# Kernel optimization log

Measured on AMD Instinct MI355X. Metric: run time of the kernel, lower is better.

The kernel has to match this reference:

```python
import jax, jax.numpy as jnp
import numpy as np

DIM = 8          # per-head dim
ATT_EPS = 1e-15  # LiteMLA eps
BN_EPS = 1e-5    # torch BatchNorm2d default eps


def conv2d(x, w, groups=1, pad=0):
    # x: NCHW, w: OIHW
    return jax.lax.conv_general_dilated(
        x, w, window_strides=(1, 1), padding=[(pad, pad), (pad, pad)],
        dimension_numbers=('NCHW', 'OIHW', 'NCHW'), feature_group_count=groups)


def setup_inputs() -> dict:
    key = jax.random.key(0)
    ks = jax.random.split(key, 6)
    B, C, H, W = 4, 128, 128, 128
    heads = C // DIM            # 16
    t3 = 3 * C                  # 3*total_dim = 384
    x = jax.random.normal(ks[0], (B, C, H, W), jnp.float32)
    w_qkv = jax.random.normal(ks[1], (t3, C, 1, 1), jnp.float32) * 0.02
    w_dw = jax.random.normal(ks[2], (t3, 1, 5, 5), jnp.float32) * 0.02      # depthwise 5x5
    w_pw = jax.random.normal(ks[3], (t3, t3 // (3 * heads), 1, 1), jnp.float32) * 0.05  # grouped 1x1, groups=3*heads
    w_proj = jax.random.normal(ks[4], (C, 2 * C, 1, 1), jnp.float32) * 0.02  # proj 1x1: 2C -> C
    bn_gamma = jnp.ones((C,), jnp.float32)
    bn_beta = jnp.zeros((C,), jnp.float32)
    bn_mean = jnp.zeros((C,), jnp.float32)
    bn_var = jnp.ones((C,), jnp.float32)
    return dict(x=x, w_qkv=w_qkv, w_dw=w_dw, w_pw=w_pw, w_proj=w_proj,
                bn_gamma=bn_gamma, bn_beta=bn_beta, bn_mean=bn_mean, bn_var=bn_var)


def reference(x, w_qkv, w_dw, w_pw, w_proj, bn_gamma, bn_beta, bn_mean, bn_var):
    # qkv: 1x1 conv, no norm / no act
    qkv = conv2d(x, w_qkv)                                  # (B, 3C, H, W)
    t3 = w_qkv.shape[0]
    # aggreg[0]: depthwise 5x5 + grouped 1x1
    groups_pw = t3 // w_pw.shape[1]                         # 3*heads
    agg = conv2d(conv2d(qkv, w_dw, groups=t3, pad=2), w_pw, groups=groups_pw)
    qkv = jnp.concatenate([qkv, agg], axis=1)               # (B, 6C, H, W)

    B, _, H, W = qkv.shape
    N = H * W
    qkv = qkv.reshape(B, -1, 3 * DIM, N)                    # (B, 2*heads, 3*dim, N)
    q = jax.nn.relu(qkv[:, :, :DIM])                        # (B, h, d, N)
    k = jax.nn.relu(qkv[:, :, DIM:2 * DIM])                 # (B, h, d, N)
    v = qkv[:, :, 2 * DIM:]                                 # (B, h, d, N)
    # pad v with a row of ones for normalization
    v = jnp.concatenate([v, jnp.ones_like(v[:, :, :1])], axis=2)  # (B, h, d+1, N)

    vk = jnp.einsum('bhdn,bhen->bhde', v, k)                # (B, h, d+1, d)
    out = jnp.einsum('bhde,bhen->bhdn', vk, q)              # (B, h, d+1, N)
    out = out[:, :, :-1] / (out[:, :, -1:] + ATT_EPS)       # (B, h, d, N)
    out = out.reshape(B, -1, H, W)                          # (B, 2C, H, W)

    # proj: 1x1 conv + BatchNorm2d (inference), no act
    out = conv2d(out, w_proj)                               # (B, C, H, W)
    inv = bn_gamma / jnp.sqrt(bn_var + BN_EPS)
    out = out * inv[:, None, None] + (bn_beta - bn_mean * inv)[:, None, None]
    return out
```

## Files before the change

### kernel.cpp

```cpp
#include <hip/hip_runtime.h>

#define BB 4
#define CIN 128
#define T3 384
#define HH 128
#define WW 128
#define NPIX 16384
#define QKV_ELE (BB*T3*NPIX)

#define SEC 4160
#define KGP 1040
#define PLN 520

typedef __attribute__((ext_vector_type(8))) short bf16x8;
typedef __attribute__((ext_vector_type(4))) float f32x4;

__device__ __forceinline__ unsigned splitpack(float x) {
  unsigned u = __float_as_uint(x);
  unsigned hb = (u + 0x7fffu + ((u >> 16) & 1u)) >> 16;
  float lo = x - __uint_as_float(hb << 16);
  unsigned ul = __float_as_uint(lo);
  unsigned lb = (ul + 0x7fffu + ((ul >> 16) & 1u)) >> 16;
  return (hb << 16) | (lb & 0xffffu);
}

__device__ __forceinline__ void packpair(float a, float b, unsigned& hi, unsigned& lo) {
  unsigned p0 = splitpack(a), p1 = splitpack(b);
  hi = (p1 & 0xffff0000u) | (p0 >> 16);
  lo = (p1 << 16) | (p0 & 0xffffu);
}

__global__ __launch_bounds__(256) void k0_wprep(const float* __restrict__ wqkv,
                                                unsigned* __restrict__ wimg,
                                                float* __restrict__ zbuf) {
  int id = blockIdx.x * 256 + threadIdx.x;
  if (id < 16) zbuf[id] = 0.f;
  int i = id & 3;
  int co = (id >> 2) & 127;
  int kgrp = (id >> 9) & 3;
  int c = (id >> 11) & 3;
  int m = id >> 13;
  int ci = c * 32 + kgrp * 8 + 2 * i;
  const float* wrow = wqkv + (size_t)(m * 128 + co) * 128 + ci;
  unsigned hi, lo;
  packpair(wrow[0], wrow[1], hi, lo);
  size_t base = (size_t)(m * 4 + c) * SEC + kgrp * KGP + co * 4 + i;
  wimg[base] = hi;
  wimg[base + PLN] = lo;
}

__global__ __launch_bounds__(256) void k1_qkv_mfma(const float* __restrict__ x,
                                                   const unsigned* __restrict__ wimg,
                                                   float* __restrict__ qkv) {
  __shared__ __align__(16) unsigned Xp[4 * KGP];
  __shared__ __align__(16) unsigned Wp[4 * KGP];
  const int t = threadIdx.x;
  const int p = blockIdx.x;
  const int qd = p / 24;
  const int r_ = p - qd * 24;
  const int m = r_ >> 3;
  const int tt = qd * 8 + (r_ & 7);
  const int n0 = (tt & 127) * 128;
  const int b = tt >> 7;
  const float* xb = x + (size_t)b * CIN * NPIX + n0;

  const int l = t & 63;
  const int w = t >> 6;
  const int g = l >> 4;
  const int lc = l & 15;
  const int ch = w >> 1;
  const int nh = w & 1;
  const int kg = t >> 6;
  const int nn_ = t & 63;

  f32x4 acc[4][4];
  #pragma unroll
  for (int i = 0; i < 4; ++i)
    #pragma unroll
    for (int j = 0; j < 4; ++j) acc[i][j] = (f32x4){0.f, 0.f, 0.f, 0.f};

  for (int c = 0; c < 4; ++c) {
    {
      const uint4* wsrc = (const uint4*)(wimg + (size_t)(m * 4 + c) * SEC);
      uint4* wdst = (uint4*)Wp;
      #pragma unroll
      for (int r = 0; r < 5; ++r) {
        int idx = t + r * 256;
        if (idx < 1040) wdst[idx] = wsrc[idx];
      }
    }
    {
      const float* colbase = xb + (size_t)(c * 32 + kg * 8) * NPIX;
      #pragma unroll
      for (int half = 0; half < 2; ++half) {
        int n = nn_ + half * 64;
        const float* colp = colbase + n;
        unsigned hp[4], lp[4];
        #pragma unroll
        for (int i = 0; i < 4; ++i)
          packpair(colp[(size_t)(2 * i) * NPIX], colp[(size_t)(2 * i + 1) * NPIX],
                   hp[i], lp[i]);
        *(uint4*)&Xp[kg * KGP + n * 4] = make_uint4(hp[0], hp[1], hp[2], hp[3]);
        *(uint4*)&Xp[kg * KGP + PLN + n * 4] = make_uint4(lp[0], lp[1], lp[2], lp[3]);
      }
    }
    __syncthreads();

    bf16x8 bh[4], bl[4];
    #pragma unroll
    for (int ng = 0; ng < 4; ++ng) {
      const int nb = (nh * 64 + ng * 16 + lc) * 4;
      bh[ng] = *(const bf16x8*)&Xp[g * KGP + nb];
      bl[ng] = *(const bf16x8*)&Xp[g * KGP + PLN + nb];
    }
    #pragma unroll
    for (int cg = 0; cg < 4; ++cg) {
      const int cb = (ch * 64 + cg * 16 + lc) * 4;
      bf16x8 ah = *(const bf16x8*)&Wp[g * KGP + cb];
      bf16x8 al = *(const bf16x8*)&Wp[g * KGP + PLN + cb];
      #pragma unroll
      for (int ng = 0; ng < 4; ++ng) {
        acc[cg][ng] = __builtin_amdgcn_mfma_f32_16x16x32_bf16(ah, bh[ng], acc[cg][ng], 0, 0, 0);
        acc[cg][ng] = __builtin_amdgcn_mfma_f32_16x16x32_bf16(ah, bl[ng], acc[cg][ng], 0, 0, 0);
        acc[cg][ng] = __builtin_amdgcn_mfma_f32_16x16x32_bf16(al, bh[ng], acc[cg][ng], 0, 0, 0);
      }
    }
    __syncthreads();
  }
  #pragma unroll
  for (int cg = 0; cg < 4; ++cg) {
    const size_t corow = (size_t)b * T3 + m * 128 + ch * 64 + cg * 16 + g * 4;
    #pragma unroll
    for (int ng = 0; ng < 4; ++ng) {
      const int nn = n0 + nh * 64 + ng * 16 + lc;
      #pragma unroll
      for (int rr = 0; rr < 4; ++rr)
        qkv[(corow + rr) * NPIX + nn] = acc[cg][ng][rr];
    }
  }
}

#define PDW 36

__device__ __forceinline__ void dw_compute(const float* __restrict__ plane,
                                           const float* __restrict__ w25,
                                           const float* __restrict__ zbuf,
                                           int x0, int y0, int xq, int yg,
                                           float dacc[4][4]) {
  const int gx0 = x0 + 4 * xq - 4;
  const bool ex0 = (gx0 >= 0);
  const bool ex2 = (gx0 + 11 < WW);
  f32x4 u[8][3];
  #pragma unroll
  for (int r = 0; r < 8; ++r) {
    const int gy = y0 + 4 * yg - 2 + r;
    const bool iny = (unsigned)gy < (unsigned)HH;
    const float* rp = plane + gy * WW + gx0;
    const float* p0 = (iny && ex0) ? rp : zbuf;
    const float* p1 = iny ? (rp + 4) : zbuf;
    const float* p2 = (iny && ex2) ? (rp + 8) : zbuf;
    u[r][0] = *(const f32x4*)p0;
    u[r][1] = *(const f32x4*)p1;
    u[r][2] = *(const f32x4*)p2;
  }
  #pragma unroll
  for (int jy = 0; jy < 4; ++jy)
    #pragma unroll
    for (int jx = 0; jx < 4; ++jx) dacc[jy][jx] = 0.f;
  #pragma unroll
  for (int r = 0; r < 8; ++r) {
    float vals[12] = {u[r][0][0], u[r][0][1], u[r][0][2], u[r][0][3],
                      u[r][1][0], u[r][1][1], u[r][1][2], u[r][1][3],
                      u[r][2][0], u[r][2][1], u[r][2][2], u[r][2][3]};
    #pragma unroll
    for (int jy = 0; jy < 4; ++jy) {
      int ky = r - jy;
      if (ky < 0 || ky > 4) continue;
      #pragma unroll
      for (int kx = 0; kx < 5; ++kx) {
        float wv = w25[ky * 5 + kx];
        #pragma unroll
        for (int jx = 0; jx < 4; ++jx)
          dacc[jy][jx] += wv * vals[jx + kx + 2];
      }
    }
  }
}

__device__ __forceinline__ void vk_reduce(const float* __restrict__ kb,
                                          const float* __restrict__ vb,
                                          float* __restrict__ pr, int t) {
  const int wv = t >> 6;
  const int lane = t & 63;
  const int d0 = wv * 2;
  float accA[8], accB[8], accS[8];
  #pragma unroll
  for (int e = 0; e < 8; ++e) { accA[e] = 0.f; accB[e] = 0.f; accS[e] = 0.f; }
  #pragma unroll
  for (int it = 0; it < 8; ++it) {
    int p = it * 64 + lane;
    float kv[8];
    #pragma unroll
    for (int e = 0; e < 8; ++e) kv[e] = kb[e * 512 + p];
    float vA = vb[d0 * 512 + p];
    float vB = vb[(d0 + 1) * 512 + p];
    #pragma unroll
    for (int e = 0; e < 8; ++e) { accA[e] += vA * kv[e]; accB[e] += vB * kv[e]; }
    if (wv == 0) {
      #pragma unroll
      for (int e = 0; e < 8; ++e) accS[e] += kv[e];
    }
  }
  #pragma unroll
  for (int e = 0; e < 8; ++e) {
    #pragma unroll
    for (int m = 1; m < 64; m <<= 1) {
      accA[e] += __shfl_xor(accA[e], m);
      accB[e] += __shfl_xor(accB[e], m);
    }
  }
  if (wv == 0) {
    #pragma unroll
    for (int e = 0; e < 8; ++e)
      #pragma unroll
      for (int m = 1; m < 64; m <<= 1) accS[e] += __shfl_xor(accS[e], m);
  }
  if (lane == 0) {
    #pragma unroll
    for (int e = 0; e < 8; ++e) {
      pr[d0 * 8 + e] = accA[e];
      pr[(d0 + 1) * 8 + e] = accB[e];
    }
    if (wv == 0) {
      #pragma unroll
      for (int e = 0; e < 8; ++e) pr[64 + e] = accS[e];
    }
  }
}

__global__ __launch_bounds__(256, 2) void k2_fused(const float* __restrict__ qkv,
                                                   const float* __restrict__ wdw,
                                                   const float* __restrict__ wpw,
                                                   const float* __restrict__ zbuf,
                                                   float* __restrict__ agg,
                                                   float* __restrict__ part2) {
  __shared__ __align__(16) float dwsv[8 * 16 * PDW];
  __shared__ __align__(16) float kbuf[8 * 512];
  __shared__ float wds[24][25];
  __shared__ float wps[192];
  const int t = threadIdx.x;
  const int p = blockIdx.x;
  const int L = (p & 7) * 256 + (p >> 3);
  const int z = L >> 5;
  const int rem = L & 31;
  const int x0 = (rem & 3) * 32;
  const int y0 = (rem >> 2) * 16;
  const int b = z >> 4;
  const int hh = z & 15;
  const float* src = qkv + ((size_t)b * T3 + hh * 24) * NPIX;

  for (int idx = t; idx < 600; idx += 256)
    wds[idx / 25][idx % 25] = wdw[(size_t)hh * 600 + idx];
  if (t < 192) wps[t] = wpw[hh * 192 + t];
  __syncthreads();

  const int ch = t >> 5;
  const int xq = t & 7;
  const int yg = (t >> 3) & 3;
  float dacc[4][4];

  dw_compute(src + (size_t)(8 + ch) * NPIX, &wds[8 + ch][0], zbuf, x0, y0, xq, yg, dacc);
  #pragma unroll
  for (int jy = 0; jy < 4; ++jy)
    *(float4*)&dwsv[ch * (16 * PDW) + (yg * 4 + jy) * PDW + xq * 4] =
        make_float4(dacc[jy][0], dacc[jy][1], dacc[jy][2], dacc[jy][3]);
  __syncthreads();
  #pragma unroll
  for (int pp = 0; pp < 2; ++pp) {
    int pix = t + pp * 256;
    int py = pix >> 5, px = pix & 31;
    float dv[8];
    #pragma unroll
    for (int ic = 0; ic < 8; ++ic) dv[ic] = dwsv[ic * (16 * PDW) + py * PDW + px];
    #pragma unroll
    for (int oc = 0; oc < 8; ++oc) {
      float s = 0.f;
      #pragma unroll
      for (int ic = 0; ic < 8; ++ic) s += wps[64 + oc * 8 + ic] * dv[ic];
      kbuf[oc * 512 + pix] = fmaxf(s, 0.f);
    }
  }
  __syncthreads();

  dw_compute(src + (size_t)(16 + ch) * NPIX, &wds[16 + ch][0], zbuf, x0, y0, xq, yg, dacc);
  #pragma unroll
  for (int jy = 0; jy < 4; ++jy)
    *(float4*)&dwsv[ch * (16 * PDW) + (yg * 4 + jy) * PDW + xq * 4] =
        make_float4(dacc[jy][0], dacc[jy][1], dacc[jy][2], dacc[jy][3]);
  __syncthreads();
  float vout[2][8];
  #pragma unroll
  for (int pp = 0; pp < 2; ++pp) {
    int pix = t + pp * 256;
    int py = pix >> 5, px = pix & 31;
    float dv[8];
    #pragma unroll
    for (int ic = 0; ic < 8; ++ic) dv[ic] = dwsv[ic * (16 * PDW) + py * PDW + px];
    #pragma unroll
    for (int oc = 0; oc < 8; ++oc) {
      float s = 0.f;
      #pragma unroll
      for (int ic = 0; ic < 8; ++ic) s += wps[128 + oc * 8 + ic] * dv[ic];
      vout[pp][oc] = s;
    }
  }
  __syncthreads();
  #pragma unroll
  for (int pp = 0; pp < 2; ++pp) {
    int pix = t + pp * 256;
    #pragma unroll
    for (int oc = 0; oc < 8; ++oc) dwsv[oc * 512 + pix] = vout[pp][oc];
  }
  __syncthreads();

  vk_reduce(kbuf, dwsv, part2 + ((size_t)(z * 2 + 1) * 32 + rem) * 72, t);
  __syncthreads();

  #pragma unroll
  for (int j = 0; j < 8; ++j) {
    int qd = t + j * 256;
    int buf = qd >> 10;
    int ch2 = (qd >> 7) & 7;
    int r2 = qd & 127;
    int py = r2 >> 3, qx = r2 & 7;
    const float* gp = src + (size_t)(8 + buf * 8 + ch2) * NPIX + (y0 + py) * WW + x0 + qx * 4;
    f32x4 v = *(const f32x4*)gp;
    if (buf == 0) {
      v[0] = fmaxf(v[0], 0.f); v[1] = fmaxf(v[1], 0.f);
      v[2] = fmaxf(v[2], 0.f); v[3] = fmaxf(v[3], 0.f);
      *(f32x4*)&kbuf[ch2 * 512 + py * 32 + qx * 4] = v;
    } else {
      *(f32x4*)&dwsv[ch2 * 512 + py * 32 + qx * 4] = v;
    }
  }
  __syncthreads();

  vk_reduce(kbuf, dwsv, part2 + ((size_t)(z * 2 + 0) * 32 + rem) * 72, t);
  __syncthreads();

  dw_compute(src + (size_t)ch * NPIX, &wds[ch][0], zbuf, x0, y0, xq, yg, dacc);
  #pragma unroll
  for (int jy = 0; jy < 4; ++jy)
    *(float4*)&dwsv[ch * (16 * PDW) + (yg * 4 + jy) * PDW + xq * 4] =
        make_float4(dacc[jy][0], dacc[jy][1], dacc[jy][2], dacc[jy][3]);
  __syncthreads();
  float* dst = agg + ((size_t)b * T3 + hh * 24) * NPIX + (size_t)y0 * WW + x0;
  #pragma unroll
  for (int pp = 0; pp < 2; ++pp) {
    int pix = t + pp * 256;
    int py = pix >> 5, px = pix & 31;
    float dv[8];
    #pragma unroll
    for (int ic = 0; ic < 8; ++ic) dv[ic] = dwsv[ic * (16 * PDW) + py * PDW + px];
    #pragma unroll
    for (int oc = 0; oc < 8; ++oc) {
      float s = 0.f;
      #pragma unroll
      for (int ic = 0; ic < 8; ++ic) s += wps[oc * 8 + ic] * dv[ic];
      dst[(size_t)oc * NPIX + py * WW + px] = s;
    }
  }
}

__global__ __launch_bounds__(128) void k3b_sum(const float* __restrict__ part2,
                                               float* __restrict__ vk) {
  const int bh = blockIdx.x;
  const int j = threadIdx.x;
  if (j < 72) {
    int b = bh >> 5, h = bh & 31;
    int z = b * 16 + (h & 15);
    int ph = h >> 4;
    const float* srcp = part2 + ((size_t)(z * 2 + ph) * 32) * 72 + j;
    float s = 0.f;
    #pragma unroll
    for (int c = 0; c < 32; ++c) s += srcp[(size_t)c * 72];
    vk[(size_t)bh * 72 + j] = s;
  }
}

__global__ __launch_bounds__(256) void k3c_M(const float* __restrict__ wproj,
                                             const float* __restrict__ vk,
                                             const float* __restrict__ gamma,
                                             const float* __restrict__ beta,
                                             const float* __restrict__ mean,
                                             const float* __restrict__ var,
                                             unsigned* __restrict__ Mimg,
                                             float* __restrict__ shiftb) {
  int id = blockIdx.x * 256 + threadIdx.x;
  int i = id & 3;
  int co = (id >> 2) & 127;
  int kgrp = (id >> 9) & 3;
  int cidx = (id >> 11) & 7;
  int b = id >> 14;
  int h = cidx * 4 + kgrp;
  float inv = gamma[co] * rsqrtf(var[co] + 1e-5f);
  const float* wrow = wproj + (size_t)co * 256 + h * 8;
  const float* vkc = vk + ((size_t)b * 32 + h) * 72;
  float s0 = 0.f, s1 = 0.f;
  #pragma unroll
  for (int d = 0; d < 8; ++d) {
    float wv = wrow[d];
    s0 += wv * vkc[d * 8 + 2 * i];
    s1 += wv * vkc[d * 8 + 2 * i + 1];
  }
  unsigned hi, lo;
  packpair(inv * s0, inv * s1, hi, lo);
  size_t base = (size_t)(b * 8 + cidx) * SEC + kgrp * KGP + co * 4 + i;
  Mimg[base] = hi;
  Mimg[base + PLN] = lo;
  if (b == 0 && cidx == 0 && kgrp == 0 && i == 0)
    shiftb[co] = beta[co] - mean[co] * inv;
}

__global__ __launch_bounds__(256) void k4_mfma(const float* __restrict__ qkv,
                                               const float* __restrict__ agg,
                                               const float* __restrict__ vk,
                                               const unsigned* __restrict__ Mimg,
                                               const float* __restrict__ shiftb,
                                               float* __restrict__ out) {
  __shared__ __align__(16) unsigned Ap[4 * KGP];
  __shared__ __align__(16) unsigned Bp[4 * KGP];
  const int t = threadIdx.x;
  const int n0 = blockIdx.x * 128;
  const int b = blockIdx.y;

  const int l = t & 63;
  const int w = t >> 6;
  const int g = l >> 4;
  const int lc = l & 15;
  const int ch = w >> 1;
  const int nh = w & 1;
  const int hj = t >> 6;
  const int nn_ = t & 63;

  f32x4 acc[4][4];
  #pragma unroll
  for (int i = 0; i < 4; ++i)
    #pragma unroll
    for (int j = 0; j < 4; ++j) acc[i][j] = (f32x4){0.f, 0.f, 0.f, 0.f};

  for (int cidx = 0; cidx < 8; ++cidx) {
    {
      const uint4* asrc = (const uint4*)(Mimg + (size_t)(b * 8 + cidx) * SEC);
      uint4* adst = (uint4*)Ap;
      #pragma unroll
      for (int r = 0; r < 5; ++r) {
        int idx = t + r * 256;
        if (idx < 1040) adst[idx] = asrc[idx];
      }
    }
    {
      const int h = cidx * 4 + hj;
      const float* srcb = (h < 16 ? qkv : agg) +
                          ((size_t)b * T3 + (h & 15) * 24) * NPIX + n0;
      const float* vkr = vk + ((size_t)b * 32 + h) * 72 + 64;
      float vv[8];
      #pragma unroll
      for (int e = 0; e < 8; ++e) vv[e] = vkr[e];
      #pragma unroll
      for (int half = 0; half < 2; ++half) {
        int n = nn_ + half * 64;
        float q[8];
        float den = 1e-15f;
        #pragma unroll
        for (int e = 0; e < 8; ++e) {
          q[e] = fmaxf(srcb[(size_t)e * NPIX + n], 0.f);
          den += vv[e] * q[e];
        }
        float rd = 1.0f / den;
        unsigned hp[4], lp[4];
        #pragma unroll
        for (int i = 0; i < 4; ++i)
          packpair(q[2 * i] * rd, q[2 * i + 1] * rd, hp[i], lp[i]);
        *(uint4*)&Bp[hj * KGP + n * 4] = make_uint4(hp[0], hp[1], hp[2], hp[3]);
        *(uint4*)&Bp[hj * KGP + PLN + n * 4] = make_uint4(lp[0], lp[1], lp[2], lp[3]);
      }
    }
    __syncthreads();

    bf16x8 bh[4], bl[4];
    #pragma unroll
    for (int ng = 0; ng < 4; ++ng) {
      const int nb = (nh * 64 + ng * 16 + lc) * 4;
      bh[ng] = *(const bf16x8*)&Bp[g * KGP + nb];
      bl[ng] = *(const bf16x8*)&Bp[g * KGP + PLN + nb];
    }
    #pragma unroll
    for (int cg = 0; cg < 4; ++cg) {
      const int cb = (ch * 64 + cg * 16 + lc) * 4;
      bf16x8 ah = *(const bf16x8*)&Ap[g * KGP + cb];
      bf16x8 al = *(const bf16x8*)&Ap[g * KGP + PLN + cb];
      #pragma unroll
      for (int ng = 0; ng < 4; ++ng) {
        acc[cg][ng] = __builtin_amdgcn_mfma_f32_16x16x32_bf16(ah, bh[ng], acc[cg][ng], 0, 0, 0);
        acc[cg][ng] = __builtin_amdgcn_mfma_f32_16x16x32_bf16(ah, bl[ng], acc[cg][ng], 0, 0, 0);
        acc[cg][ng] = __builtin_amdgcn_mfma_f32_16x16x32_bf16(al, bh[ng], acc[cg][ng], 0, 0, 0);
      }
    }
    __syncthreads();
  }
  #pragma unroll
  for (int cg = 0; cg < 4; ++cg) {
    const int cobase = ch * 64 + cg * 16 + g * 4;
    #pragma unroll
    for (int ng = 0; ng < 4; ++ng) {
      const int nn = n0 + nh * 64 + ng * 16 + lc;
      #pragma unroll
      for (int rr = 0; rr < 4; ++rr) {
        int co = cobase + rr;
        out[((size_t)b * 128 + co) * NPIX + nn] = acc[cg][ng][rr] + shiftb[co];
      }
    }
  }
}

__global__ void fill_sentinel(float* o, int n) {
  int i = blockIdx.x * 256 + threadIdx.x;
  if (i < n) o[i] = 12345.0f;
}

extern "C" void kernel_launch(void* const* d_in, const int* in_sizes, int n_in,
                              void* d_out, int out_size, void* d_ws, size_t ws_size,
                              hipStream_t stream) {
  const float* x     = (const float*)d_in[0];
  const float* wqkv  = (const float*)d_in[1];
  const float* wdw   = (const float*)d_in[2];
  const float* wpw   = (const float*)d_in[3];
  const float* wproj = (const float*)d_in[4];
  const float* gamma = (const float*)d_in[5];
  const float* beta  = (const float*)d_in[6];
  const float* mean  = (const float*)d_in[7];
  const float* var   = (const float*)d_in[8];
  float* out = (float*)d_out;
  float* ws = (float*)d_ws;

  const size_t part2F = 64 * 2 * 32 * 72;
  const size_t mimgF = 32 * SEC;
  const size_t wimgF = 12 * SEC;
  const size_t needF = (size_t)QKV_ELE * 2 + part2F + 9216 + 128 + mimgF + wimgF + 16;
  if (ws_size < needF * 4) {
    fill_sentinel<<<dim3((out_size + 255) / 256), dim3(256), 0, stream>>>(out, out_size);
    return;
  }
  float* qkv    = ws;
  float* agg    = qkv + QKV_ELE;
  float* part2  = agg + QKV_ELE;
  float* vkbuf  = part2 + part2F;
  float* shiftb = vkbuf + 9216;
  unsigned* Mimg = (unsigned*)(shiftb + 128);
  unsigned* wimg = Mimg + mimgF;
  float* zbuf   = (float*)(wimg + wimgF);

  k0_wprep<<<dim3(96), 256, 0, stream>>>(wqkv, wimg, zbuf);
  k1_qkv_mfma<<<dim3(1536), 256, 0, stream>>>(x, wimg, qkv);
  k2_fused<<<dim3(2048), 256, 0, stream>>>(qkv, wdw, wpw, zbuf, agg, part2);
  k3b_sum<<<dim3(128), 128, 0, stream>>>(part2, vkbuf);
  k3c_M<<<dim3(256), 256, 0, stream>>>(wproj, vkbuf, gamma, beta, mean, var, Mimg, shiftb);
  k4_mfma<<<dim3(128, 4), 256, 0, stream>>>(qkv, agg, vkbuf, Mimg, shiftb, out);
}
```

Before: 146.5 us.

## Batch K and V depthwise passes, prefetch raw K/V, raise occupancy hint

The fused aggregation kernel now computes the K and V depthwise convolutions back to back into two shared buffers, then runs both grouped 1x1 projections in one pass. This removes several barriers and exposes more independent loads. The raw K/V tile for the second reduction is loaded into registers before the first vk_reduce so its global latency overlaps that reduction. The launch bound minimum blocks per CU is raised from 2 to 4, which raises register pressure from the extra live arrays (rs, kout, vout) and risks spills.

```diff
diff --git a/kernel.cpp b/kernel.cpp
--- a/kernel.cpp
+++ b/kernel.cpp
@@ -238,14 +238,14 @@
   }
 }
 
-__global__ __launch_bounds__(256, 2) void k2_fused(const float* __restrict__ qkv,
+__global__ __launch_bounds__(256, 4) void k2_fused(const float* __restrict__ qkv,
                                                    const float* __restrict__ wdw,
                                                    const float* __restrict__ wpw,
                                                    const float* __restrict__ zbuf,
                                                    float* __restrict__ agg,
                                                    float* __restrict__ part2) {
-  __shared__ __align__(16) float dwsv[8 * 16 * PDW];
-  __shared__ __align__(16) float kbuf[8 * 512];
+  __shared__ __align__(16) float bufA[8 * 16 * PDW];
+  __shared__ __align__(16) float bufB[8 * 16 * PDW];
   __shared__ float wds[24][25];
   __shared__ float wps[192];
   const int t = threadIdx.x;
@@ -267,101 +267,109 @@
   const int ch = t >> 5;
   const int xq = t & 7;
   const int yg = (t >> 3) & 3;
-  float dacc[4][4];
-
-  dw_compute(src + (size_t)(8 + ch) * NPIX, &wds[8 + ch][0], zbuf, x0, y0, xq, yg, dacc);
-  #pragma unroll
-  for (int jy = 0; jy < 4; ++jy)
-    *(float4*)&dwsv[ch * (16 * PDW) + (yg * 4 + jy) * PDW + xq * 4] =
-        make_float4(dacc[jy][0], dacc[jy][1], dacc[jy][2], dacc[jy][3]);
-  __syncthreads();
+
+  {
+    float daccK[4][4], daccV[4][4];
+    dw_compute(src + (size_t)(8 + ch) * NPIX, &wds[8 + ch][0], zbuf, x0, y0, xq, yg, daccK);
+    dw_compute(src + (size_t)(16 + ch) * NPIX, &wds[16 + ch][0], zbuf, x0, y0, xq, yg, daccV);
+    #pragma unroll
+    for (int jy = 0; jy < 4; ++jy) {
+      *(float4*)&bufA[ch * (16 * PDW) + (yg * 4 + jy) * PDW + xq * 4] =
+          make_float4(daccK[jy][0], daccK[jy][1], daccK[jy][2], daccK[jy][3]);
+      *(float4*)&bufB[ch * (16 * PDW) + (yg * 4 + jy) * PDW + xq * 4] =
+          make_float4(daccV[jy][0], daccV[jy][1], daccV[jy][2], daccV[jy][3]);
+    }
+  }
+  __syncthreads();
+
+  float kout[2][8], vout[2][8];
+  #pragma unroll
+  for (int pp = 0; pp < 2; ++pp) {
+    int pix = t + pp * 256;
+    int py = pix >> 5, px = pix & 31;
+    float dvA[8], dvB[8];
+    #pragma unroll
+    for (int ic = 0; ic < 8; ++ic) {
+      dvA[ic] = bufA[ic * (16 * PDW) + py * PDW + px];
+      dvB[ic] = bufB[ic * (16 * PDW) + py * PDW + px];
+    }
+    #pragma unroll
+    for (int oc = 0; oc < 8; ++oc) {
+      float sk = 0.f, sv = 0.f;
+      #pragma unroll
+      for (int ic = 0; ic < 8; ++ic) {
+        sk += wps[64 + oc * 8 + ic] * dvA[ic];
+        sv += wps[128 + oc * 8 + ic] * dvB[ic];
+      }
+      kout[pp][oc] = sk;
+      vout[pp][oc] = sv;
+    }
+  }
+  __syncthreads();
+
+  #pragma unroll
+  for (int pp = 0; pp < 2; ++pp) {
+    int pix = t + pp * 256;
+    #pragma unroll
+    for (int oc = 0; oc < 8; ++oc) {
+      bufA[oc * 512 + pix] = fmaxf(kout[pp][oc], 0.f);
+      bufB[oc * 512 + pix] = vout[pp][oc];
+    }
+  }
+  __syncthreads();
+
+  f32x4 rs[8];
+  #pragma unroll
+  for (int j = 0; j < 8; ++j) {
+    int qd2 = t + j * 256;
+    int buf = qd2 >> 10;
+    int ch2 = (qd2 >> 7) & 7;
+    int r2 = qd2 & 127;
+    int py = r2 >> 3, qx = r2 & 7;
+    const float* gp = src + (size_t)(8 + buf * 8 + ch2) * NPIX + (y0 + py) * WW + x0 + qx * 4;
+    rs[j] = *(const f32x4*)gp;
+  }
+  vk_reduce(bufA, bufB, part2 + ((size_t)(z * 2 + 1) * 32 + rem) * 72, t);
+  __syncthreads();
+
+  #pragma unroll
+  for (int j = 0; j < 8; ++j) {
+    int qd2 = t + j * 256;
+    int buf = qd2 >> 10;
+    int ch2 = (qd2 >> 7) & 7;
+    int r2 = qd2 & 127;
+    int py = r2 >> 3, qx = r2 & 7;
+    f32x4 v = rs[j];
+    if (buf == 0) {
+      v[0] = fmaxf(v[0], 0.f); v[1] = fmaxf(v[1], 0.f);
+      v[2] = fmaxf(v[2], 0.f); v[3] = fmaxf(v[3], 0.f);
+      *(f32x4*)&bufA[ch2 * 512 + py * 32 + qx * 4] = v;
+    } else {
+      *(f32x4*)&bufB[ch2 * 512 + py * 32 + qx * 4] = v;
+    }
+  }
+  __syncthreads();
+
+  vk_reduce(bufA, bufB, part2 + ((size_t)(z * 2 + 0) * 32 + rem) * 72, t);
+  __syncthreads();
+
+  {
+    float dacc[4][4];
+    dw_compute(src + (size_t)ch * NPIX, &wds[ch][0], zbuf, x0, y0, xq, yg, dacc);
+    #pragma unroll
+    for (int jy = 0; jy < 4; ++jy)
+      *(float4*)&bufA[ch * (16 * PDW) + (yg * 4 + jy) * PDW + xq * 4] =
+          make_float4(dacc[jy][0], dacc[jy][1], dacc[jy][2], dacc[jy][3]);
+  }
+  __syncthreads();
+  float* dst = agg + ((size_t)b * T3 + hh * 24) * NPIX + (size_t)y0 * WW + x0;
   #pragma unroll
   for (int pp = 0; pp < 2; ++pp) {
     int pix = t + pp * 256;
     int py = pix >> 5, px = pix & 31;
     float dv[8];
     #pragma unroll
-    for (int ic = 0; ic < 8; ++ic) dv[ic] = dwsv[ic * (16 * PDW) + py * PDW + px];
-    #pragma unroll
-    for (int oc = 0; oc < 8; ++oc) {
-      float s = 0.f;
-      #pragma unroll
-      for (int ic = 0; ic < 8; ++ic) s += wps[64 + oc * 8 + ic] * dv[ic];
-      kbuf[oc * 512 + pix] = fmaxf(s, 0.f);
-    }
-  }
-  __syncthreads();
-
-  dw_compute(src + (size_t)(16 + ch) * NPIX, &wds[16 + ch][0], zbuf, x0, y0, xq, yg, dacc);
-  #pragma unroll
-  for (int jy = 0; jy < 4; ++jy)
-    *(float4*)&dwsv[ch * (16 * PDW) + (yg * 4 + jy) * PDW + xq * 4] =
-        make_float4(dacc[jy][0], dacc[jy][1], dacc[jy][2], dacc[jy][3]);
-  __syncthreads();
-  float vout[2][8];
-  #pragma unroll
-  for (int pp = 0; pp < 2; ++pp) {
-    int pix = t + pp * 256;
-    int py = pix >> 5, px = pix & 31;
-    float dv[8];
-    #pragma unroll
-    for (int ic = 0; ic < 8; ++ic) dv[ic] = dwsv[ic * (16 * PDW) + py * PDW + px];
-    #pragma unroll
-    for (int oc = 0; oc < 8; ++oc) {
-      float s = 0.f;
-      #pragma unroll
-      for (int ic = 0; ic < 8; ++ic) s += wps[128 + oc * 8 + ic] * dv[ic];
-      vout[pp][oc] = s;
-    }
-  }
-  __syncthreads();
-  #pragma unroll
-  for (int pp = 0; pp < 2; ++pp) {
-    int pix = t + pp * 256;
-    #pragma unroll
-    for (int oc = 0; oc < 8; ++oc) dwsv[oc * 512 + pix] = vout[pp][oc];
-  }
-  __syncthreads();
-
-  vk_reduce(kbuf, dwsv, part2 + ((size_t)(z * 2 + 1) * 32 + rem) * 72, t);
-  __syncthreads();
-
-  #pragma unroll
-  for (int j = 0; j < 8; ++j) {
-    int qd = t + j * 256;
-    int buf = qd >> 10;
-    int ch2 = (qd >> 7) & 7;
-    int r2 = qd & 127;
-    int py = r2 >> 3, qx = r2 & 7;
-    const float* gp = src + (size_t)(8 + buf * 8 + ch2) * NPIX + (y0 + py) * WW + x0 + qx * 4;
-    f32x4 v = *(const f32x4*)gp;
-    if (buf == 0) {
-      v[0] = fmaxf(v[0], 0.f); v[1] = fmaxf(v[1], 0.f);
-      v[2] = fmaxf(v[2], 0.f); v[3] = fmaxf(v[3], 0.f);
-      *(f32x4*)&kbuf[ch2 * 512 + py * 32 + qx * 4] = v;
-    } else {
-      *(f32x4*)&dwsv[ch2 * 512 + py * 32 + qx * 4] = v;
-    }
-  }
-  __syncthreads();
-
-  vk_reduce(kbuf, dwsv, part2 + ((size_t)(z * 2 + 0) * 32 + rem) * 72, t);
-  __syncthreads();
-
-  dw_compute(src + (size_t)ch * NPIX, &wds[ch][0], zbuf, x0, y0, xq, yg, dacc);
-  #pragma unroll
-  for (int jy = 0; jy < 4; ++jy)
-    *(float4*)&dwsv[ch * (16 * PDW) + (yg * 4 + jy) * PDW + xq * 4] =
-        make_float4(dacc[jy][0], dacc[jy][1], dacc[jy][2], dacc[jy][3]);
-  __syncthreads();
-  float* dst = agg + ((size_t)b * T3 + hh * 24) * NPIX + (size_t)y0 * WW + x0;
-  #pragma unroll
-  for (int pp = 0; pp < 2; ++pp) {
-    int pix = t + pp * 256;
-    int py = pix >> 5, px = pix & 31;
-    float dv[8];
-    #pragma unroll
-    for (int ic = 0; ic < 8; ++ic) dv[ic] = dwsv[ic * (16 * PDW) + py * PDW + px];
+    for (int ic = 0; ic < 8; ++ic) dv[ic] = bufA[ic * (16 * PDW) + py * PDW + px];
     #pragma unroll
     for (int oc = 0; oc < 8; ++oc) {
       float s = 0.f;
```

New measurement: 160.3 us. 1.09x slower.
